# Kernel optimization log

Hardware: AMD Instinct MI355X
Metric: run time of the kernel (lower is better)

## Reference

```python
import jax, jax.numpy as jnp
import numpy as np

# CrossAttention (DFFNet): 1x1 convs produce q,k from depth and v from rgb;
# full dense attention over hw spatial tokens: softmax(q^T k) then v @ mask^T.

def setup_inputs() -> dict:
    key = jax.random.key(0)
    ks = jax.random.split(key, 8)
    B, C, H, W = 4, 256, 64, 64
    Cqk = C // 8  # ratio=8 -> 32
    s = 0.02
    return {
        "rgb":   jax.random.normal(ks[0], (B, C, H, W), jnp.float32),
        "depth": jax.random.normal(ks[1], (B, C, H, W), jnp.float32),
        "Wq": jax.random.normal(ks[2], (Cqk, C), jnp.float32) * s,
        "bq": jax.random.normal(ks[3], (Cqk,), jnp.float32) * s,
        "Wk": jax.random.normal(ks[4], (Cqk, C), jnp.float32) * s,
        "bk": jax.random.normal(ks[5], (Cqk,), jnp.float32) * s,
        "Wv": jax.random.normal(ks[6], (C, C), jnp.float32) * s,
        "bv": jax.random.normal(ks[7], (C,), jnp.float32) * s,
    }


def reference(rgb, depth, Wq, bq, Wk, bk, Wv, bv):
    B, C, H, W = rgb.shape
    hw = H * W
    d = depth.reshape(B, C, hw)   # [B, C, hw]
    r = rgb.reshape(B, C, hw)     # [B, C, hw]
    # 1x1 convs == channel-mixing linear maps
    q = jnp.einsum('oc,bcn->bon', Wq, d) + bq[None, :, None]  # [B, Cqk, hw]
    k = jnp.einsum('oc,bcn->bon', Wk, d) + bk[None, :, None]  # [B, Cqk, hw]
    v = jnp.einsum('oc,bcn->bon', Wv, r) + bv[None, :, None]  # [B, C, hw]
    # scores: q^T k -> [B, hw, hw], softmax over last dim
    scores = jnp.einsum('bcn,bcm->bnm', q, k)
    mask = jax.nn.softmax(scores, axis=-1)
    # feat = v @ mask^T  -> [B, C, hw]
    feat = jnp.einsum('bcm,bnm->bcn', v, mask)
    return feat.reshape(B, C, H, W)
```

## Files before the change

### kernel.cpp

```cpp
#include <hip/hip_runtime.h>
#include <stdint.h>

#define L2E 1.44269504088896340736f

typedef _Float16 half8 __attribute__((ext_vector_type(8)));
typedef float floatx4 __attribute__((ext_vector_type(4)));

static __device__ __forceinline__ unsigned short f32_to_f16u(float f) {
  union { _Float16 h; unsigned short s; } cv; cv.h = (_Float16)f; return cv.s;
}

__global__ __launch_bounds__(256) void proj_kernel(
    const float* __restrict__ rgb,
    const float* __restrict__ depth,
    const float* __restrict__ Wq, const float* __restrict__ bq,
    const float* __restrict__ Wk, const float* __restrict__ bk,
    const float* __restrict__ Wv, const float* __restrict__ bv,
    unsigned short* __restrict__ qT,
    unsigned short* __restrict__ kT,
    unsigned short* __restrict__ v)
{
  __shared__ __align__(16) unsigned short sW[64 * 256];

  const int n0 = blockIdx.x * 64;
  const int b  = blockIdx.y;
  const int z  = blockIdx.z;
  const int t  = threadIdx.x;
  const int w  = t >> 6;
  const int lane = t & 63;
  const int l15 = lane & 15;
  const int q4  = lane >> 4;

  const float* X = (z == 0) ? depth : rgb;
  const float* xb = X + (size_t)b * 256 * 4096;
  const int n_row = n0 + 16 * w + l15;
  const int colbase = (z == 0) ? 0 : (z - 1) * 64;

#pragma unroll
  for (int it = 0; it < 8; it++) {
    int L = it * 256 + t;
    int og = L >> 5;
    int phys = L & 31;
    int ci = phys ^ (og & 7);
    const float* wr;
    if (z == 0) wr = (og < 32) ? (Wq + (size_t)og * 256) : (Wk + (size_t)(og - 32) * 256);
    else        wr = Wv + (size_t)(colbase + og) * 256;
    float4 w0 = *(const float4*)(wr + ci * 8);
    float4 w1 = *(const float4*)(wr + ci * 8 + 4);
    half8 h;
    h[0] = (_Float16)w0.x; h[1] = (_Float16)w0.y; h[2] = (_Float16)w0.z; h[3] = (_Float16)w0.w;
    h[4] = (_Float16)w1.x; h[5] = (_Float16)w1.y; h[6] = (_Float16)w1.z; h[7] = (_Float16)w1.w;
    *(half8*)&sW[(size_t)L * 8] = h;
  }

  float bias[4];
#pragma unroll
  for (int ct = 0; ct < 4; ct++) {
    int og = ct * 16 + l15;
    if (z == 0) bias[ct] = (og < 32) ? bq[og] : bk[og - 32];
    else        bias[ct] = bv[colbase + og];
  }
  __syncthreads();

  floatx4 acc[4];
#pragma unroll
  for (int i = 0; i < 4; i++) acc[i] = (floatx4){0.f, 0.f, 0.f, 0.f};

#pragma unroll
  for (int ks = 0; ks < 8; ks++) {
    const int c0 = ks * 32;
    half8 a;
#pragma unroll
    for (int j = 0; j < 8; j++) {
      int c = c0 + q4 * 8 + j;
      a[j] = (_Float16)xb[(size_t)c * 4096 + n_row];
    }
    const int ci = ks * 4 + q4;
#pragma unroll
    for (int ct = 0; ct < 4; ct++) {
      int og = ct * 16 + l15;
      half8 bf = *(const half8*)&sW[og * 256 + ((ci ^ (og & 7)) * 8)];
      acc[ct] = __builtin_amdgcn_mfma_f32_16x16x32_f16(a, bf, acc[ct], 0, 0, 0);
    }
  }

  __syncthreads();

  if (z == 0) {
#pragma unroll
    for (int ct = 0; ct < 4; ct++) {
      int og = ct * 16 + l15;
#pragma unroll
      for (int r = 0; r < 4; r++) {
        int n = n0 + 16 * w + q4 * 4 + r;
        unsigned short hv = f32_to_f16u(acc[ct][r] + bias[ct]);
        if (og < 32) qT[((size_t)b * 4096 + n) * 32 + og] = hv;
        else         kT[((size_t)b * 4096 + n) * 32 + (og - 32)] = hv;
      }
    }
  } else {
    unsigned short* tile = sW;
#pragma unroll
    for (int ct = 0; ct < 4; ct++) {
#pragma unroll
      for (int r = 0; r < 4; r++) {
        int co_l = ct * 16 + l15;
        int nl = 16 * w + q4 * 4 + r;
        tile[co_l * 72 + nl] = f32_to_f16u(acc[ct][r] + bias[ct]);
      }
    }
    __syncthreads();
#pragma unroll
    for (int it = 0; it < 2; it++) {
      int co_l = it * 32 + (t >> 3);
      int ch = t & 7;
      int4 val = *(const int4*)&tile[co_l * 72 + ch * 8];
      *(int4*)&v[((size_t)b * 256 + colbase + co_l) * 4096 + n0 + ch * 8] = val;
    }
  }
}

__global__ __launch_bounds__(256, 4) void attn_kernel(
    const unsigned short* __restrict__ qT,
    const unsigned short* __restrict__ kT,
    const unsigned short* __restrict__ v,
    unsigned short* __restrict__ Op,
    float* __restrict__ lW)
{
  __shared__ __align__(16) unsigned char smem[36864];
  unsigned short* sV = (unsigned short*)smem;
  unsigned short* sK = (unsigned short*)(smem + 16384);
  unsigned short* sP = (unsigned short*)(smem + 18432);

  const int n0 = blockIdx.x * 64;
  const int b  = blockIdx.y;
  const int chunk = blockIdx.z;
  const int t  = threadIdx.x;
  const int w  = t >> 6;
  const int lane = t & 63;
  const int l15 = lane & 15;
  const int q4  = lane >> 4;

  const unsigned short* qrow = qT + ((size_t)b * 4096 + n0 + 16 * w + l15) * 32 + q4 * 8;
  half8 aq = *(const half8*)qrow;

  const unsigned short* vB = v  + (size_t)b * 256 * 4096;
  const unsigned short* kB = kT + (size_t)b * 4096 * 32;
  unsigned short* sPw = sP + w * 640;

  float lsum[4] = {0.f, 0.f, 0.f, 0.f};
  floatx4 acc[16];
#pragma unroll
  for (int ct = 0; ct < 16; ct++) acc[ct] = (floatx4){0.f, 0.f, 0.f, 0.f};
  const floatx4 zf = (floatx4){0.f, 0.f, 0.f, 0.f};

  const int mbase = chunk * 1024;
  for (int mi = 0; mi < 1024; mi += 32) {
    const int m0 = mbase + mi;
    __syncthreads();
#pragma unroll
    for (int j = 0; j < 4; j++) {
      int lin = j * 256 + t;
      int c = lin >> 2;
      int p = lin & 3;
      int lc = p ^ ((c >> 1) & 3);
      uint4 val = *(const uint4*)&vB[(size_t)c * 4096 + m0 + lc * 8];
      *(uint4*)&sV[lin * 8] = val;
    }
    if (t < 128) {
      int m = t >> 2, p = t & 3, lc = p ^ ((m >> 1) & 3);
      uint4 val = *(const uint4*)&kB[(size_t)(m0 + m) * 32 + lc * 8];
      *(uint4*)&sK[t * 8] = val;
    }
    __syncthreads();

    half8 bk0 = *(const half8*)&sK[l15 * 32 + ((q4 ^ ((l15 >> 1) & 3)) * 8)];
    half8 bk1 = *(const half8*)&sK[(16 + l15) * 32 + ((q4 ^ (((16 + l15) >> 1) & 3)) * 8)];
    floatx4 s0 = __builtin_amdgcn_mfma_f32_16x16x32_f16(aq, bk0, zf, 0, 0, 0);
    floatx4 s1 = __builtin_amdgcn_mfma_f32_16x16x32_f16(aq, bk1, zf, 0, 0, 0);

    float p0[4], p1[4];
#pragma unroll
    for (int r = 0; r < 4; r++) {
      p0[r] = exp2f(s0[r] * L2E);
      p1[r] = exp2f(s1[r] * L2E);
      lsum[r] += p0[r] + p1[r];
    }
#pragma unroll
    for (int r = 0; r < 4; r++) {
      int row = q4 * 4 + r;
      sPw[row * 40 + l15]      = f32_to_f16u(p0[r]);
      sPw[row * 40 + 16 + l15] = f32_to_f16u(p1[r]);
    }
    asm volatile("s_waitcnt lgkmcnt(0)" ::: "memory");
    half8 ap = *(const half8*)&sPw[l15 * 40 + q4 * 8];
#pragma unroll
    for (int ct = 0; ct < 16; ct++) {
      int co = ct * 16 + l15;
      half8 bv8 = *(const half8*)&sV[co * 32 + ((q4 ^ ((co >> 1) & 3)) * 8)];
      acc[ct] = __builtin_amdgcn_mfma_f32_16x16x32_f16(ap, bv8, acc[ct], 0, 0, 0);
    }
  }

#pragma unroll
  for (int off = 1; off < 16; off <<= 1) {
#pragma unroll
    for (int r = 0; r < 4; r++) lsum[r] += __shfl_xor(lsum[r], off);
  }
  if (l15 == 0) {
#pragma unroll
    for (int r = 0; r < 4; r++)
      lW[((size_t)chunk * 4 + b) * 4096 + n0 + 16 * w + q4 * 4 + r] = lsum[r];
  }

  unsigned short* sO = (unsigned short*)smem;
#pragma unroll
  for (int pass = 0; pass < 2; pass++) {
    __syncthreads();
#pragma unroll
    for (int cl = 0; cl < 8; cl++) {
      int ct = pass * 8 + cl;
      int co_l = cl * 16 + l15;
#pragma unroll
      for (int r = 0; r < 4; r++) {
        int nl = 16 * w + q4 * 4 + r;
        sO[co_l * 72 + nl] = f32_to_f16u(acc[ct][r]);
      }
    }
    __syncthreads();
#pragma unroll
    for (int s = 0; s < 4; s++) {
      int co_l = s * 32 + (t >> 3);
      int ch = t & 7;
      int4 val = *(const int4*)&sO[co_l * 72 + ch * 8];
      *(int4*)&Op[(((size_t)chunk * 4 + b) * 256 + pass * 128 + co_l) * 4096 + n0 + ch * 8] = val;
    }
  }
}

__global__ __launch_bounds__(256) void combine_kernel(
    const unsigned short* __restrict__ Op,
    const float* __restrict__ lW,
    float* __restrict__ out)
{
  const int t = threadIdx.x;
  const int b = blockIdx.y;
  const size_t n8 = (size_t)blockIdx.x * 2048 + (size_t)t * 8;
  const int co0 = blockIdx.z * 8;

  float sum[8] = {0.f, 0.f, 0.f, 0.f, 0.f, 0.f, 0.f, 0.f};
#pragma unroll
  for (int ch = 0; ch < 4; ch++) {
    const float* lp = lW + ((size_t)ch * 4 + b) * 4096 + n8;
    float4 a0 = *(const float4*)lp;
    float4 a1 = *(const float4*)(lp + 4);
    sum[0] += a0.x; sum[1] += a0.y; sum[2] += a0.z; sum[3] += a0.w;
    sum[4] += a1.x; sum[5] += a1.y; sum[6] += a1.z; sum[7] += a1.w;
  }
  float rl[8];
#pragma unroll
  for (int i = 0; i < 8; i++) rl[i] = 1.0f / sum[i];

#pragma unroll
  for (int cc = 0; cc < 8; cc++) {
    int co = co0 + cc;
    float o[8] = {0.f, 0.f, 0.f, 0.f, 0.f, 0.f, 0.f, 0.f};
#pragma unroll
    for (int ch = 0; ch < 4; ch++) {
      half8 hv = *(const half8*)&Op[(((size_t)ch * 4 + b) * 256 + co) * 4096 + n8];
#pragma unroll
      for (int i = 0; i < 8; i++) o[i] += (float)hv[i];
    }
    float* op = out + ((size_t)b * 256 + co) * 4096 + n8;
    float4 r0, r1;
    r0.x = o[0] * rl[0]; r0.y = o[1] * rl[1]; r0.z = o[2] * rl[2]; r0.w = o[3] * rl[3];
    r1.x = o[4] * rl[4]; r1.y = o[5] * rl[5]; r1.z = o[6] * rl[6]; r1.w = o[7] * rl[7];
    *(float4*)op = r0;
    *(float4*)(op + 4) = r1;
  }
}

extern "C" void kernel_launch(void* const* d_in, const int* in_sizes, int n_in,
                              void* d_out, int out_size, void* d_ws, size_t ws_size,
                              hipStream_t stream) {
  const float* rgb   = (const float*)d_in[0];
  const float* depth = (const float*)d_in[1];
  const float* Wq    = (const float*)d_in[2];
  const float* bq    = (const float*)d_in[3];
  const float* Wk    = (const float*)d_in[4];
  const float* bk    = (const float*)d_in[5];
  const float* Wv    = (const float*)d_in[6];
  const float* bv    = (const float*)d_in[7];
  float* out = (float*)d_out;

  unsigned short* qT = (unsigned short*)d_ws;
  unsigned short* kT = qT + (size_t)4 * 4096 * 32;
  unsigned short* vW = kT + (size_t)4 * 4096 * 32;
  unsigned short* Op = vW + (size_t)4 * 256 * 4096;
  float* lW = (float*)(Op + (size_t)4 * 4 * 256 * 4096);

  dim3 pg(64, 4, 5);
  proj_kernel<<<pg, 256, 0, stream>>>(rgb, depth, Wq, bq, Wk, bk, Wv, bv, qT, kT, vW);
  dim3 ag(64, 4, 4);
  attn_kernel<<<ag, 256, 0, stream>>>(qT, kT, vW, Op, lW);
  dim3 cg(2, 4, 32);
  combine_kernel<<<cg, 256, 0, stream>>>(Op, lW, out);
}
```

Baseline: 172.0 us.

## Use 32x32 MFMA tiles in attention PV and merge V projection blocks

The attention PV product now shares the P tile across all four waves through shared memory. Each wave owns 64 output channels and uses 32x32x16 MFMA instructions, where before each wave computed all 256 channels for its own 16 rows with 16x16 MFMAs. This cuts V-fragment reads from LDS per MFMA and lowers instruction count, at the cost of an extra block-wide barrier per key step. The V projection also now computes all 256 output channels in one block instead of four, so each rgb element is read once rather than four times. The weights are streamed through LDS per k-slice, with the next activation slice prefetched, in exchange for more barriers and fewer blocks.

```diff
diff --git a/kernel.cpp b/kernel.cpp
--- a/kernel.cpp
+++ b/kernel.cpp
@@ -5,12 +5,14 @@
 
 typedef _Float16 half8 __attribute__((ext_vector_type(8)));
 typedef float floatx4 __attribute__((ext_vector_type(4)));
+typedef float floatx16 __attribute__((ext_vector_type(16)));
 
 static __device__ __forceinline__ unsigned short f32_to_f16u(float f) {
   union { _Float16 h; unsigned short s; } cv; cv.h = (_Float16)f; return cv.s;
 }
-
-__global__ __launch_bounds__(256) void proj_kernel(
+static __device__ __forceinline__ _Float16 f32h(float f) { return (_Float16)f; }
+
+__global__ __launch_bounds__(256, 2) void proj_kernel(
     const float* __restrict__ rgb,
     const float* __restrict__ depth,
     const float* __restrict__ Wq, const float* __restrict__ bq,
@@ -30,63 +32,50 @@
   const int lane = t & 63;
   const int l15 = lane & 15;
   const int q4  = lane >> 4;
-
-  const float* X = (z == 0) ? depth : rgb;
-  const float* xb = X + (size_t)b * 256 * 4096;
   const int n_row = n0 + 16 * w + l15;
-  const int colbase = (z == 0) ? 0 : (z - 1) * 64;
-
-#pragma unroll
-  for (int it = 0; it < 8; it++) {
-    int L = it * 256 + t;
-    int og = L >> 5;
-    int phys = L & 31;
-    int ci = phys ^ (og & 7);
-    const float* wr;
-    if (z == 0) wr = (og < 32) ? (Wq + (size_t)og * 256) : (Wk + (size_t)(og - 32) * 256);
-    else        wr = Wv + (size_t)(colbase + og) * 256;
-    float4 w0 = *(const float4*)(wr + ci * 8);
-    float4 w1 = *(const float4*)(wr + ci * 8 + 4);
-    half8 h;
-    h[0] = (_Float16)w0.x; h[1] = (_Float16)w0.y; h[2] = (_Float16)w0.z; h[3] = (_Float16)w0.w;
-    h[4] = (_Float16)w1.x; h[5] = (_Float16)w1.y; h[6] = (_Float16)w1.z; h[7] = (_Float16)w1.w;
-    *(half8*)&sW[(size_t)L * 8] = h;
-  }
-
-  float bias[4];
-#pragma unroll
-  for (int ct = 0; ct < 4; ct++) {
-    int og = ct * 16 + l15;
-    if (z == 0) bias[ct] = (og < 32) ? bq[og] : bk[og - 32];
-    else        bias[ct] = bv[colbase + og];
-  }
-  __syncthreads();
-
-  floatx4 acc[4];
-#pragma unroll
-  for (int i = 0; i < 4; i++) acc[i] = (floatx4){0.f, 0.f, 0.f, 0.f};
-
-#pragma unroll
-  for (int ks = 0; ks < 8; ks++) {
-    const int c0 = ks * 32;
-    half8 a;
-#pragma unroll
-    for (int j = 0; j < 8; j++) {
-      int c = c0 + q4 * 8 + j;
-      a[j] = (_Float16)xb[(size_t)c * 4096 + n_row];
-    }
-    const int ci = ks * 4 + q4;
+
+  if (z == 0) {
+    const float* xb = depth + (size_t)b * 256 * 4096;
+#pragma unroll
+    for (int it = 0; it < 8; it++) {
+      int L = it * 256 + t;
+      int og = L >> 5;
+      int phys = L & 31;
+      int ci = phys ^ (og & 7);
+      const float* wr = (og < 32) ? (Wq + (size_t)og * 256) : (Wk + (size_t)(og - 32) * 256);
+      float4 w0 = *(const float4*)(wr + ci * 8);
+      float4 w1 = *(const float4*)(wr + ci * 8 + 4);
+      half8 h;
+      h[0] = f32h(w0.x); h[1] = f32h(w0.y); h[2] = f32h(w0.z); h[3] = f32h(w0.w);
+      h[4] = f32h(w1.x); h[5] = f32h(w1.y); h[6] = f32h(w1.z); h[7] = f32h(w1.w);
+      *(half8*)&sW[(size_t)L * 8] = h;
+    }
+    float bias[4];
 #pragma unroll
     for (int ct = 0; ct < 4; ct++) {
       int og = ct * 16 + l15;
-      half8 bf = *(const half8*)&sW[og * 256 + ((ci ^ (og & 7)) * 8)];
-      acc[ct] = __builtin_amdgcn_mfma_f32_16x16x32_f16(a, bf, acc[ct], 0, 0, 0);
-    }
-  }
-
-  __syncthreads();
-
-  if (z == 0) {
+      bias[ct] = (og < 32) ? bq[og] : bk[og - 32];
+    }
+    __syncthreads();
+
+    floatx4 acc[4];
+#pragma unroll
+    for (int i = 0; i < 4; i++) acc[i] = (floatx4){0.f, 0.f, 0.f, 0.f};
+#pragma unroll
+    for (int ks = 0; ks < 8; ks++) {
+      const int c0 = ks * 32;
+      half8 a;
+#pragma unroll
+      for (int j = 0; j < 8; j++)
+        a[j] = (_Float16)xb[(size_t)(c0 + q4 * 8 + j) * 4096 + n_row];
+      const int ci = ks * 4 + q4;
+#pragma unroll
+      for (int ct = 0; ct < 4; ct++) {
+        int og = ct * 16 + l15;
+        half8 bf = *(const half8*)&sW[og * 256 + ((ci ^ (og & 7)) * 8)];
+        acc[ct] = __builtin_amdgcn_mfma_f32_16x16x32_f16(a, bf, acc[ct], 0, 0, 0);
+      }
+    }
 #pragma unroll
     for (int ct = 0; ct < 4; ct++) {
       int og = ct * 16 + l15;
@@ -99,23 +88,75 @@
       }
     }
   } else {
+    const float* xb = rgb + (size_t)b * 256 * 4096;
+    float bias[16];
+#pragma unroll
+    for (int ct = 0; ct < 16; ct++) bias[ct] = bv[ct * 16 + l15];
+
+    floatx4 acc[16];
+#pragma unroll
+    for (int ct = 0; ct < 16; ct++) acc[ct] = (floatx4){0.f, 0.f, 0.f, 0.f};
+
+    half8 a_cur;
+#pragma unroll
+    for (int j = 0; j < 8; j++)
+      a_cur[j] = (_Float16)xb[(size_t)(q4 * 8 + j) * 4096 + n_row];
+
+    for (int ks = 0; ks < 8; ks++) {
+      const int c0 = ks * 32;
+      __syncthreads();
+#pragma unroll
+      for (int u = 0; u < 4; u++) {
+        int L = u * 256 + t;
+        int o = L >> 2;
+        int p = L & 3;
+        int ci = p ^ (o & 3);
+        const float* wr = Wv + (size_t)o * 256 + c0 + ci * 8;
+        float4 w0 = *(const float4*)wr;
+        float4 w1 = *(const float4*)(wr + 4);
+        half8 h;
+        h[0] = f32h(w0.x); h[1] = f32h(w0.y); h[2] = f32h(w0.z); h[3] = f32h(w0.w);
+        h[4] = f32h(w1.x); h[5] = f32h(w1.y); h[6] = f32h(w1.z); h[7] = f32h(w1.w);
+        *(half8*)&sW[(size_t)L * 8] = h;
+      }
+      __syncthreads();
+      half8 a_nxt = a_cur;
+      if (ks < 7) {
+#pragma unroll
+        for (int j = 0; j < 8; j++)
+          a_nxt[j] = (_Float16)xb[(size_t)(c0 + 32 + q4 * 8 + j) * 4096 + n_row];
+      }
+#pragma unroll
+      for (int ct = 0; ct < 16; ct++) {
+        int o = ct * 16 + l15;
+        half8 bf = *(const half8*)&sW[(o * 4 + (q4 ^ (o & 3))) * 8];
+        acc[ct] = __builtin_amdgcn_mfma_f32_16x16x32_f16(a_cur, bf, acc[ct], 0, 0, 0);
+      }
+      a_cur = a_nxt;
+    }
+
     unsigned short* tile = sW;
 #pragma unroll
-    for (int ct = 0; ct < 4; ct++) {
-#pragma unroll
-      for (int r = 0; r < 4; r++) {
-        int co_l = ct * 16 + l15;
-        int nl = 16 * w + q4 * 4 + r;
-        tile[co_l * 72 + nl] = f32_to_f16u(acc[ct][r] + bias[ct]);
-      }
-    }
-    __syncthreads();
-#pragma unroll
-    for (int it = 0; it < 2; it++) {
-      int co_l = it * 32 + (t >> 3);
-      int ch = t & 7;
-      int4 val = *(const int4*)&tile[co_l * 72 + ch * 8];
-      *(int4*)&v[((size_t)b * 256 + colbase + co_l) * 4096 + n0 + ch * 8] = val;
+    for (int pass = 0; pass < 4; pass++) {
+      __syncthreads();
+#pragma unroll
+      for (int cc = 0; cc < 4; cc++) {
+        int ct = pass * 4 + cc;
+        int co_l = cc * 16 + l15;
+#pragma unroll
+        for (int r = 0; r < 4; r++) {
+          int nl = 16 * w + q4 * 4 + r;
+          tile[co_l * 72 + nl] = f32_to_f16u(acc[ct][r] + bias[ct]);
+        }
+      }
+      __syncthreads();
+#pragma unroll
+      for (int it = 0; it < 2; it++) {
+        int co_l = it * 32 + (t >> 3);
+        int ch = t & 7;
+        int4 val = *(const int4*)&tile[co_l * 72 + ch * 8];
+        *(int4*)&v[((size_t)b * 256 + pass * 64 + co_l) * 4096 + n0 + ch * 8] = val;
+      }
     }
   }
 }
@@ -140,18 +181,23 @@
   const int lane = t & 63;
   const int l15 = lane & 15;
   const int q4  = lane >> 4;
+  const int l31 = lane & 31;
+  const int hi  = lane >> 5;
 
   const unsigned short* qrow = qT + ((size_t)b * 4096 + n0 + 16 * w + l15) * 32 + q4 * 8;
   half8 aq = *(const half8*)qrow;
 
   const unsigned short* vB = v  + (size_t)b * 256 * 4096;
   const unsigned short* kB = kT + (size_t)b * 4096 * 32;
-  unsigned short* sPw = sP + w * 640;
 
   float lsum[4] = {0.f, 0.f, 0.f, 0.f};
-  floatx4 acc[16];
-#pragma unroll
-  for (int ct = 0; ct < 16; ct++) acc[ct] = (floatx4){0.f, 0.f, 0.f, 0.f};
+  floatx16 acc[2][2];
+#pragma unroll
+  for (int nt = 0; nt < 2; nt++)
+#pragma unroll
+    for (int ct = 0; ct < 2; ct++)
+#pragma unroll
+      for (int i = 0; i < 16; i++) acc[nt][ct][i] = 0.f;
   const floatx4 zf = (floatx4){0.f, 0.f, 0.f, 0.f};
 
   const int mbase = chunk * 1024;
@@ -188,17 +234,29 @@
     }
 #pragma unroll
     for (int r = 0; r < 4; r++) {
-      int row = q4 * 4 + r;
-      sPw[row * 40 + l15]      = f32_to_f16u(p0[r]);
-      sPw[row * 40 + 16 + l15] = f32_to_f16u(p1[r]);
-    }
-    asm volatile("s_waitcnt lgkmcnt(0)" ::: "memory");
-    half8 ap = *(const half8*)&sPw[l15 * 40 + q4 * 8];
-#pragma unroll
-    for (int ct = 0; ct < 16; ct++) {
-      int co = ct * 16 + l15;
-      half8 bv8 = *(const half8*)&sV[co * 32 + ((q4 ^ ((co >> 1) & 3)) * 8)];
-      acc[ct] = __builtin_amdgcn_mfma_f32_16x16x32_f16(ap, bv8, acc[ct], 0, 0, 0);
+      int row = w * 16 + q4 * 4 + r;
+      sP[row * 40 + l15]      = f32_to_f16u(p0[r]);
+      sP[row * 40 + 16 + l15] = f32_to_f16u(p1[r]);
+    }
+    __syncthreads();
+
+#pragma unroll
+    for (int kst = 0; kst < 2; kst++) {
+      half8 bvv[2];
+#pragma unroll
+      for (int ct = 0; ct < 2; ct++) {
+        int co = w * 64 + ct * 32 + l31;
+        int lc = (kst * 2 + hi) ^ ((co >> 1) & 3);
+        bvv[ct] = *(const half8*)&sV[(co * 4 + lc) * 8];
+      }
+#pragma unroll
+      for (int nt = 0; nt < 2; nt++) {
+        half8 ap = *(const half8*)&sP[(nt * 32 + l31) * 40 + kst * 16 + hi * 8];
+#pragma unroll
+        for (int ct = 0; ct < 2; ct++) {
+          acc[nt][ct] = __builtin_amdgcn_mfma_f32_32x32x16_f16(ap, bvv[ct], acc[nt][ct], 0, 0, 0);
+        }
+      }
     }
   }
 
@@ -213,28 +271,32 @@
       lW[((size_t)chunk * 4 + b) * 4096 + n0 + 16 * w + q4 * 4 + r] = lsum[r];
   }
 
+  __syncthreads();
   unsigned short* sO = (unsigned short*)smem;
 #pragma unroll
-  for (int pass = 0; pass < 2; pass++) {
-    __syncthreads();
-#pragma unroll
-    for (int cl = 0; cl < 8; cl++) {
-      int ct = pass * 8 + cl;
-      int co_l = cl * 16 + l15;
-#pragma unroll
-      for (int r = 0; r < 4; r++) {
-        int nl = 16 * w + q4 * 4 + r;
-        sO[co_l * 72 + nl] = f32_to_f16u(acc[ct][r]);
-      }
-    }
-    __syncthreads();
-#pragma unroll
-    for (int s = 0; s < 4; s++) {
-      int co_l = s * 32 + (t >> 3);
-      int ch = t & 7;
-      int4 val = *(const int4*)&sO[co_l * 72 + ch * 8];
-      *(int4*)&Op[(((size_t)chunk * 4 + b) * 256 + pass * 128 + co_l) * 4096 + n0 + ch * 8] = val;
-    }
+  for (int nt = 0; nt < 2; nt++) {
+#pragma unroll
+    for (int ct = 0; ct < 2; ct++) {
+      int co_l = w * 64 + ct * 32 + l31;
+#pragma unroll
+      for (int g = 0; g < 4; g++) {
+        int nl = nt * 32 + g * 8 + hi * 4;
+        ushort4 pk;
+        pk.x = f32_to_f16u(acc[nt][ct][g * 4 + 0]);
+        pk.y = f32_to_f16u(acc[nt][ct][g * 4 + 1]);
+        pk.z = f32_to_f16u(acc[nt][ct][g * 4 + 2]);
+        pk.w = f32_to_f16u(acc[nt][ct][g * 4 + 3]);
+        *(ushort4*)&sO[co_l * 72 + nl] = pk;
+      }
+    }
+  }
+  __syncthreads();
+#pragma unroll
+  for (int s = 0; s < 8; s++) {
+    int co_l = s * 32 + (t >> 3);
+    int ch = t & 7;
+    int4 val = *(const int4*)&sO[co_l * 72 + ch * 8];
+    *(int4*)&Op[(((size_t)chunk * 4 + b) * 256 + co_l) * 4096 + n0 + ch * 8] = val;
   }
 }
 
@@ -299,7 +361,7 @@
   unsigned short* Op = vW + (size_t)4 * 256 * 4096;
   float* lW = (float*)(Op + (size_t)4 * 4 * 256 * 4096);
 
-  dim3 pg(64, 4, 5);
+  dim3 pg(64, 4, 2);
   proj_kernel<<<pg, 256, 0, stream>>>(rgb, depth, Wq, bq, Wk, bk, Wv, bv, qT, kT, vW);
   dim3 ag(64, 4, 4);
   attn_kernel<<<ag, 256, 0, stream>>>(qT, kT, vW, Op, lW);
```

Result: slower. 176.8 us (+2.7%).
